# Kernel optimization log

Hardware: AMD Instinct MI355X
Metric: run time of the kernel (lower is better)

The kernel has to match this reference:

```python
import jax, jax.numpy as jnp
import numpy as np

R = 2  # p-norm order, matches init kwarg r=2
NUM_CLASSES = 13  # hardcoded in the original forward


def setup_inputs() -> dict:
    key = jax.random.key(0)
    k1, k2, k3, k4, k5 = jax.random.split(key, 5)
    N = 262144
    inp = jax.random.uniform(k1, (N, NUM_CLASSES), dtype=jnp.float32)
    target = jax.random.randint(k2, (N,), 0, NUM_CLASSES, dtype=jnp.int64)
    s = jax.random.normal(k3, (N, NUM_CLASSES), dtype=jnp.float32)
    C_matrix = jax.random.normal(k4, (N, NUM_CLASSES, NUM_CLASSES), dtype=jnp.float32)
    instance_weights = jax.random.uniform(k5, (N,), dtype=jnp.float32)
    return {"input": inp, "target": target, "s": s, "C_matrix": C_matrix,
            "instance_weights": instance_weights}


def _pnorm(x, r, axis):
    # torch.norm(x, r, dim) for float r: (sum |x|^r)^(1/r)
    return jnp.sum(jnp.abs(x) ** r, axis=axis) ** (1.0 / r)


def reference(input, target, s, C_matrix, instance_weights):
    # one-hot scatter of targets: p[n, target[n]] = 1
    p = jax.nn.one_hot(target, NUM_CLASSES, dtype=input.dtype)  # [N,13]
    # batched matvec: C_matrix [N,13,13] @ p [N,13] -> [N,13]
    z_pe = jnp.einsum('nij,nj->ni', C_matrix, p)
    z_p = s - z_pe
    z_p_norm = _pnorm(z_p, R, axis=1)  # [N]
    z_ye = jnp.einsum('nij,nj->ni', C_matrix, input)
    z_y = s - z_ye
    z_y_norm = _pnorm(z_y, R, axis=1)  # [N]
    # diag(z_y @ z_p^T) == row-wise dot product (original wastefully builds NxN)
    diag = jnp.sum(z_y * z_p, axis=1)  # [N]
    return jnp.sum(z_p_norm - diag / z_y_norm)
```

## Files before the change

kernel.cpp:

```cpp
#include <hip/hip_runtime.h>
#include <hip/hip_bf16.h>

#define NCLS 13
#define BLOCK 256
#define GPB (BLOCK / 16)

typedef float f4 __attribute__((ext_vector_type(4), aligned(4)));

__global__ __launch_bounds__(BLOCK) void rnorm_kernel(
    const float* __restrict__ input,
    const int* __restrict__ target,
    const float* __restrict__ s,
    const float* __restrict__ C,
    float* __restrict__ out,
    int N)
{
    __shared__ float wsum[4];
    const int tid = threadIdx.x;
    const int q   = tid & 15;
    const int g   = tid >> 4;

    float res_acc = 0.0f;

    for (int row = blockIdx.x * GPB + g; row < N; row += gridDim.x * GPB) {
        float sp = 0.0f, sy = 0.0f, dd = 0.0f;
        if (q < NCLS) {
            const float* cr = C + (size_t)row * (NCLS * NCLS) + q * NCLS;
            const f4 c0 = *(const f4*)(cr);
            const f4 c1 = *(const f4*)(cr + 4);
            const f4 c2 = *(const f4*)(cr + 8);
            const float c12 = cr[12];

            const float* xr = input + (size_t)row * NCLS;
            const f4 x0 = *(const f4*)(xr);
            const f4 x1 = *(const f4*)(xr + 4);
            const f4 x2 = *(const f4*)(xr + 8);
            const float x12 = xr[12];

            const int t = target[row];

            float zye = c12 * x12;
#pragma unroll
            for (int k = 0; k < 4; ++k) {
                zye = fmaf(c0[k], x0[k], zye);
                zye = fmaf(c1[k], x1[k], zye);
                zye = fmaf(c2[k], x2[k], zye);
            }
            float zpe = c12;
#pragma unroll
            for (int k = 0; k < 4; ++k) {
                zpe = (t == k)     ? c0[k] : zpe;
                zpe = (t == k + 4) ? c1[k] : zpe;
                zpe = (t == k + 8) ? c2[k] : zpe;
            }

            const float svi = s[(size_t)row * NCLS + q];
            const float zp = svi - zpe, zy = svi - zye;
            sp = zp * zp; sy = zy * zy; dd = zy * zp;
        }

        sp += __shfl_xor(sp, 1); sp += __shfl_xor(sp, 2);
        sp += __shfl_xor(sp, 4); sp += __shfl_xor(sp, 8);
        sy += __shfl_xor(sy, 1); sy += __shfl_xor(sy, 2);
        sy += __shfl_xor(sy, 4); sy += __shfl_xor(sy, 8);
        dd += __shfl_xor(dd, 1); dd += __shfl_xor(dd, 2);
        dd += __shfl_xor(dd, 4); dd += __shfl_xor(dd, 8);

        if (q == 0)
            res_acc += sqrtf(sp) - dd / sqrtf(sy);
    }

#pragma unroll
    for (int off = 32; off > 0; off >>= 1)
        res_acc += __shfl_down(res_acc, off, 64);

    const int lane = tid & 63;
    const int wid  = tid >> 6;
    if (lane == 0) wsum[wid] = res_acc;
    __syncthreads();
    if (tid == 0)
        atomicAdd(out, wsum[0] + wsum[1] + wsum[2] + wsum[3]);
}

extern "C" void kernel_launch(void* const* d_in, const int* in_sizes, int n_in,
                              void* d_out, int out_size, void* d_ws, size_t ws_size,
                              hipStream_t stream) {
    const float* input  = (const float*)d_in[0];
    const int*   target = (const int*)d_in[1];
    const float* s      = (const float*)d_in[2];
    const float* C      = (const float*)d_in[3];

    float* out = (float*)d_out;
    int N = in_sizes[1];

    hipMemsetAsync(out, 0, sizeof(float) * out_size, stream);

    rnorm_kernel<<<2048, BLOCK, 0, stream>>>(input, target, s, C, out, N);
}
```

Baseline: 53.78 us.

## Stage C, input and s through LDS with async triple-buffered global_load_lds

Each wave now owns 64 rows and streams them in tiles of four rows through a three-deep LDS ring using global_load_lds, with manual vmcnt waits so loads for later tiles overlap compute on the current tile. The grid is sized so there is one block per 256 rows instead of a fixed grid-stride loop, and targets are loaded once per wave and distributed with shuffles. The point is to keep more memory requests in flight and make the C reads fully coalesced. In exchange it uses a lot of LDS (around 28 KB per block), which can limit occupancy, and it depends on fragile hand-written waitcnt ordering. It also assumes N is a multiple of 256.

```diff
diff --git a/kernel.cpp b/kernel.cpp
--- a/kernel.cpp
+++ b/kernel.cpp
@@ -2,59 +2,86 @@
 #include <hip/hip_bf16.h>
 
 #define NCLS 13
+#define NBUF 3
+#define RPT 4
+#define TPW 16
 #define BLOCK 256
-#define GPB (BLOCK / 16)
+#define CWT (RPT * NCLS * NCLS)
+#define XWT (RPT * NCLS)
 
-typedef float f4 __attribute__((ext_vector_type(4), aligned(4)));
+__device__ __forceinline__ void async_cp16(const float* g, float* l) {
+    __builtin_amdgcn_global_load_lds(
+        (__attribute__((address_space(1))) void*)(const_cast<float*>(g)),
+        (__attribute__((address_space(3))) void*)(l),
+        16, 0, 0);
+}
 
 __global__ __launch_bounds__(BLOCK) void rnorm_kernel(
     const float* __restrict__ input,
     const int* __restrict__ target,
     const float* __restrict__ s,
     const float* __restrict__ C,
-    float* __restrict__ out,
-    int N)
+    float* __restrict__ out)
 {
+    __shared__ __align__(16) float cbuf[4][NBUF][CWT];
+    __shared__ __align__(16) float xbuf[4][NBUF][XWT];
+    __shared__ __align__(16) float sbuf[4][NBUF][XWT];
     __shared__ float wsum[4];
-    const int tid = threadIdx.x;
-    const int q   = tid & 15;
-    const int g   = tid >> 4;
+
+    const int tid  = threadIdx.x;
+    const int w    = tid >> 6;
+    const int lane = tid & 63;
+    const int rloc = lane >> 4;
+    const int q    = lane & 15;
+
+    const int w0 = blockIdx.x * (BLOCK) + w * (RPT * TPW);
+
+    int trg = target[w0 + lane];
+    asm volatile("" : "+v"(trg));
+
+    auto stage = [&](int t_idx, int buf) {
+        const int r0 = w0 + t_idx * RPT;
+        const float4* Cg = (const float4*)(C + (size_t)r0 * (NCLS * NCLS));
+        float* cd = &cbuf[w][buf][0];
+        async_cp16((const float*)(Cg + lane),       cd + (size_t)lane * 4);
+        async_cp16((const float*)(Cg + 64 + lane),  cd + (size_t)(64 + lane) * 4);
+        if (lane < CWT / 4 - 128)
+            async_cp16((const float*)(Cg + 128 + lane), cd + (size_t)(128 + lane) * 4);
+        const float4* xg = (const float4*)(input + (size_t)r0 * NCLS);
+        if (lane < XWT / 4)
+            async_cp16((const float*)(xg + lane), &xbuf[w][buf][0] + (size_t)lane * 4);
+        const float4* sg = (const float4*)(s + (size_t)r0 * NCLS);
+        if (lane < XWT / 4)
+            async_cp16((const float*)(sg + lane), &sbuf[w][buf][0] + (size_t)lane * 4);
+    };
 
     float res_acc = 0.0f;
 
-    for (int row = blockIdx.x * GPB + g; row < N; row += gridDim.x * GPB) {
+    stage(0, 0);
+    stage(1, 1);
+    asm volatile("s_waitcnt vmcnt(5)" ::: "memory");
+    __builtin_amdgcn_sched_barrier(0);
+
+    for (int t = 0; t < TPW; ++t) {
+        const int bcur = t % NBUF;
+        if (t + 2 < TPW)
+            stage(t + 2, (t + 2) % NBUF);
+
+        const float* cbt = cbuf[w][bcur];
+        const float* xbt = xbuf[w][bcur];
+        const float* sbt = sbuf[w][bcur];
+        const int tt = __shfl(trg, t * RPT + rloc);
+
         float sp = 0.0f, sy = 0.0f, dd = 0.0f;
         if (q < NCLS) {
-            const float* cr = C + (size_t)row * (NCLS * NCLS) + q * NCLS;
-            const f4 c0 = *(const f4*)(cr);
-            const f4 c1 = *(const f4*)(cr + 4);
-            const f4 c2 = *(const f4*)(cr + 8);
-            const float c12 = cr[12];
-
-            const float* xr = input + (size_t)row * NCLS;
-            const f4 x0 = *(const f4*)(xr);
-            const f4 x1 = *(const f4*)(xr + 4);
-            const f4 x2 = *(const f4*)(xr + 8);
-            const float x12 = xr[12];
-
-            const int t = target[row];
-
-            float zye = c12 * x12;
+            const float* crow = cbt + rloc * (NCLS * NCLS) + q * NCLS;
+            const float* xrow = xbt + rloc * NCLS;
+            float zye = 0.0f;
 #pragma unroll
-            for (int k = 0; k < 4; ++k) {
-                zye = fmaf(c0[k], x0[k], zye);
-                zye = fmaf(c1[k], x1[k], zye);
-                zye = fmaf(c2[k], x2[k], zye);
-            }
-            float zpe = c12;
-#pragma unroll
-            for (int k = 0; k < 4; ++k) {
-                zpe = (t == k)     ? c0[k] : zpe;
-                zpe = (t == k + 4) ? c1[k] : zpe;
-                zpe = (t == k + 8) ? c2[k] : zpe;
-            }
-
-            const float svi = s[(size_t)row * NCLS + q];
+            for (int j = 0; j < NCLS; ++j)
+                zye = fmaf(crow[j], xrow[j], zye);
+            const float zpe = crow[tt];
+            const float svi = sbt[rloc * NCLS + q];
             const float zp = svi - zpe, zy = svi - zye;
             sp = zp * zp; sy = zy * zy; dd = zy * zp;
         }
@@ -68,15 +95,19 @@
 
         if (q == 0)
             res_acc += sqrtf(sp) - dd / sqrtf(sy);
+
+        if (t + 1 < TPW) {
+            if (t + 2 < TPW) asm volatile("s_waitcnt vmcnt(5)" ::: "memory");
+            else             asm volatile("s_waitcnt vmcnt(0)" ::: "memory");
+            __builtin_amdgcn_sched_barrier(0);
+        }
     }
 
 #pragma unroll
     for (int off = 32; off > 0; off >>= 1)
         res_acc += __shfl_down(res_acc, off, 64);
 
-    const int lane = tid & 63;
-    const int wid  = tid >> 6;
-    if (lane == 0) wsum[wid] = res_acc;
+    if (lane == 0) wsum[w] = res_acc;
     __syncthreads();
     if (tid == 0)
         atomicAdd(out, wsum[0] + wsum[1] + wsum[2] + wsum[3]);
@@ -95,5 +126,6 @@
 
     hipMemsetAsync(out, 0, sizeof(float) * out_size, stream);
 
-    rnorm_kernel<<<2048, BLOCK, 0, stream>>>(input, target, s, C, out, N);
+    const int grid = N / BLOCK;
+    rnorm_kernel<<<grid, BLOCK, 0, stream>>>(input, target, s, C, out);
 }
```

Measured after the change: 49.88 us. 1.08x faster.
